# Kernel tuning notes

Hardware: AMD Instinct MI355X
Metric: run time of the kernel (lower is better)

The kernel has to match this reference:

```python
import jax, jax.numpy as jnp
import numpy as np

B, C, L = 64, 64, 8192
EPS = float(np.finfo(np.float32).eps)  # matches np.finfo(np.float32).eps in the torch code


def setup_inputs() -> dict:
    key = jax.random.key(0)
    k1, k2, k3 = jax.random.split(key, 3)
    data = jax.random.normal(k1, (B, C, L), dtype=jnp.float32)
    idxes = jax.random.randint(k2, (B, L), 0, L).astype(jnp.int32)
    # prefix lengths in [1, L] so every slice is non-empty (ragged branch)
    zero_pos = jax.random.randint(k3, (B,), 1, L + 1)
    return {"data": data, "idxes": idxes, "zero_pos": zero_pos}


def reference(data, idxes, zero_pos):
    # data: [B, C, L]; per-batch mean/std over the prefix data[b, :, :zero_pos[b]]
    Bn, Cn, Ln = data.shape
    mask = (jnp.arange(Ln)[None, :] < zero_pos[:, None])[:, None, :].astype(data.dtype)  # [B,1,L]
    cnt = Cn * zero_pos.astype(data.dtype)  # [B] number of elements in each prefix
    mean = jnp.sum(data * mask, axis=(1, 2)) / cnt  # [B]
    diff = (data - mean[:, None, None]) * mask  # [B,C,L]
    var = jnp.sum(diff * diff, axis=(1, 2)) / (cnt - 1.0)  # unbiased, as torch.std
    std = jnp.sqrt(var)  # [B]
    out = (data - mean[:, None, None]) / (std[:, None, None] + EPS)
    return (out, idxes, zero_pos)
```

## Files before the change

kernel.cpp:

```cpp
#include <hip/hip_runtime.h>
#include <math.h>

#define BB 64
#define CC 64
#define LL 8192
#define EPS_F 1.1920928955078125e-07f
#define SPLITS 32

#define NORM_BLOCKS_PER_B 64
#define NB_NORM (BB * NORM_BLOCKS_PER_B)
#define NB_AUX  512

typedef float f4 __attribute__((ext_vector_type(4)));
typedef int   i4 __attribute__((ext_vector_type(4)));


__global__ __launch_bounds__(256) void tln_stats(const float* __restrict__ data,
                          const int* __restrict__ zero_pos,
                          float2* __restrict__ partials) {
    const int b = blockIdx.x;
    const int s = blockIdx.y;
    const int tid = threadIdx.x;
    const int zp = zero_pos[b];
    const int nv = zp >> 2;
    const float* base = data + (size_t)b * CC * LL;

    float sum = 0.0f, sq = 0.0f;
    for (int c = s; c < CC; c += SPLITS) {
        const float* rowp = base + (size_t)c * LL;
        const f4* row4 = (const f4*)rowp;
        for (int i = tid; i < nv; i += 256) {
            f4 v = row4[i];
            sum += v.x + v.y + v.z + v.w;
            sq  += v.x * v.x + v.y * v.y + v.z * v.z + v.w * v.w;
        }
        for (int l = (nv << 2) + tid; l < zp; l += 256) {
            float v = rowp[l];
            sum += v;
            sq  += v * v;
        }
    }

    #pragma unroll
    for (int off = 32; off > 0; off >>= 1) {
        sum += __shfl_down(sum, off);
        sq  += __shfl_down(sq, off);
    }
    __shared__ float lsum[4], lsq[4];
    const int wave = tid >> 6;
    const int lane = tid & 63;
    if (lane == 0) { lsum[wave] = sum; lsq[wave] = sq; }
    __syncthreads();
    if (tid == 0) {
        float2 p;
        p.x = lsum[0] + lsum[1] + lsum[2] + lsum[3];
        p.y = lsq[0] + lsq[1] + lsq[2] + lsq[3];
        partials[b * SPLITS + s] = p;
    }
}

__global__ __launch_bounds__(256) void tln_fused(const f4* __restrict__ data4,
                          const float2* __restrict__ partials,
                          const int* __restrict__ zero_pos,
                          const i4* __restrict__ idxes,
                          f4* __restrict__ out4,
                          f4* __restrict__ out_idx,
                          float* __restrict__ out_zp) {
    const int blk = blockIdx.x;
    const int tid = threadIdx.x;

    if (blk < NB_NORM) {
        const int b = blk >> 6;
        const int t = blk & 63;
        const int lane = tid & 63;

        float2 p = partials[(b << 5) + (lane & 31)];
        float s_ = p.x, q_ = p.y;
        #pragma unroll
        for (int off = 16; off > 0; off >>= 1) {
            s_ += __shfl_xor(s_, off);
            q_ += __shfl_xor(q_, off);
        }
        const float cnt  = (float)CC * (float)zero_pos[b];
        const float mean = s_ / cnt;
        const float var  = (q_ - cnt * mean * mean) / (cnt - 1.0f);
        const float inv  = 1.0f / (sqrtf(var) + EPS_F);

        const size_t base = ((size_t)b << 17) | ((size_t)t << 11) | (size_t)tid;
        #pragma unroll
        for (int k = 0; k < 8; ++k) {
            const size_t i = base + ((size_t)k << 8);
            f4 v = data4[i];
            f4 o = (v - mean) * inv;
            __builtin_nontemporal_store(o, out4 + i);
        }
    } else {
        const int j = blk - NB_NORM;
        const int i = j * 256 + tid;
        i4 v = idxes[i];
        f4 o = __builtin_convertvector(v, f4);
        __builtin_nontemporal_store(o, out_idx + i);
        if (j == 0 && tid < BB) out_zp[tid] = (float)zero_pos[tid];
    }
}

extern "C" void kernel_launch(void* const* d_in, const int* in_sizes, int n_in,
                              void* d_out, int out_size, void* d_ws, size_t ws_size,
                              hipStream_t stream) {
    const float* data    = (const float*)d_in[0];
    const int* idxes     = (const int*)d_in[1];
    const int* zero_pos  = (const int*)d_in[2];

    float2* partials = (float2*)d_ws;

    float* out_data = (float*)d_out;
    float* out_idx  = out_data + (size_t)BB * CC * LL;
    float* out_zp   = out_idx + (size_t)BB * LL;

    tln_stats<<<dim3(BB, SPLITS), 256, 0, stream>>>(data, zero_pos, partials);

    tln_fused<<<NB_NORM + NB_AUX, 256, 0, stream>>>(
        (const f4*)data, partials, zero_pos, (const i4*)idxes,
        (f4*)out_data, (f4*)out_idx, out_zp);
}
```

Baseline: 248.3 us.

## Fuse stats and normalize kernels into one pass with atomic per-batch barrier

Merges the statistics kernel and the normalize kernel into a single launch. Each block reduces its four-row slice, adds the partial sums to per-batch atomic accumulators, and bumps a completion flag. It then spins until all 16 blocks of its batch have reported, and normalizes the same rows it just read, which are likely still in cache. The idx conversion work is folded into the same blocks. This removes one launch and the dependency gap between kernels, at the cost of a workspace memset, float atomics, and reliance on all blocks of a batch being co-resident to avoid deadlock.

```diff
diff --git a/kernel.cpp b/kernel.cpp
--- a/kernel.cpp
+++ b/kernel.cpp
@@ -5,39 +5,54 @@
 #define CC 64
 #define LL 8192
 #define EPS_F 1.1920928955078125e-07f
-#define SPLITS 32
 
-#define NORM_BLOCKS_PER_B 64
-#define NB_NORM (BB * NORM_BLOCKS_PER_B)
-#define NB_AUX  512
+#define GROUPS 16
+#define ROWS_PER_BLK 4
+#define NBLK (BB * GROUPS)
+#define ROW4 (LL / 4)
 
 typedef float f4 __attribute__((ext_vector_type(4)));
 typedef int   i4 __attribute__((ext_vector_type(4)));
 
 
-__global__ __launch_bounds__(256) void tln_stats(const float* __restrict__ data,
-                          const int* __restrict__ zero_pos,
-                          float2* __restrict__ partials) {
-    const int b = blockIdx.x;
-    const int s = blockIdx.y;
+__global__ __launch_bounds__(256) void tln_onepass(
+    const float* __restrict__ data,
+    const int*   __restrict__ zero_pos,
+    const i4*    __restrict__ idxes,
+    float*       __restrict__ ws,
+    f4*          __restrict__ out4,
+    f4*          __restrict__ out_idx,
+    float*       __restrict__ out_zp)
+{
+    const int blk = blockIdx.x;
     const int tid = threadIdx.x;
-    const int zp = zero_pos[b];
-    const int nv = zp >> 2;
-    const float* base = data + (size_t)b * CC * LL;
+    const int b   = blk >> 4;
+    const int t   = blk & 15;
+    const int zp  = zero_pos[b];
+    const int nv  = zp >> 2;
+    const int rem = zp & 3;
+
+    float* sums  = ws;
+    float* sqs   = ws + 64;
+    int*   flags = (int*)(ws + 128);
+
+    const float* base = data + ((size_t)b * CC + (size_t)t * ROWS_PER_BLK) * LL;
 
     float sum = 0.0f, sq = 0.0f;
-    for (int c = s; c < CC; c += SPLITS) {
-        const float* rowp = base + (size_t)c * LL;
+    #pragma unroll
+    for (int r = 0; r < ROWS_PER_BLK; ++r) {
+        const float* rowp = base + (size_t)r * LL;
         const f4* row4 = (const f4*)rowp;
         for (int i = tid; i < nv; i += 256) {
             f4 v = row4[i];
             sum += v.x + v.y + v.z + v.w;
             sq  += v.x * v.x + v.y * v.y + v.z * v.z + v.w * v.w;
         }
-        for (int l = (nv << 2) + tid; l < zp; l += 256) {
-            float v = rowp[l];
-            sum += v;
-            sq  += v * v;
+        if (rem && tid == 0) {
+            for (int e = 0; e < rem; ++e) {
+                float v = rowp[nv * 4 + e];
+                sum += v; sq += v * v;
+            }
         }
     }
 
@@ -47,60 +62,56 @@
         sq  += __shfl_down(sq, off);
     }
     __shared__ float lsum[4], lsq[4];
+    __shared__ float s_m, s_inv;
     const int wave = tid >> 6;
     const int lane = tid & 63;
     if (lane == 0) { lsum[wave] = sum; lsq[wave] = sq; }
     __syncthreads();
     if (tid == 0) {
-        float2 p;
-        p.x = lsum[0] + lsum[1] + lsum[2] + lsum[3];
-        p.y = lsq[0] + lsq[1] + lsq[2] + lsq[3];
-        partials[b * SPLITS + s] = p;
+        float bs = lsum[0] + lsum[1] + lsum[2] + lsum[3];
+        float bq = lsq[0] + lsq[1] + lsq[2] + lsq[3];
+        atomicAdd(&sums[b], bs);
+        atomicAdd(&sqs[b],  bq);
+        __hip_atomic_fetch_add(&flags[b], 1, __ATOMIC_RELEASE,
+                               __HIP_MEMORY_SCOPE_AGENT);
     }
-}
 
-__global__ __launch_bounds__(256) void tln_fused(const f4* __restrict__ data4,
-                          const float2* __restrict__ partials,
-                          const int* __restrict__ zero_pos,
-                          const i4* __restrict__ idxes,
-                          f4* __restrict__ out4,
-                          f4* __restrict__ out_idx,
-                          float* __restrict__ out_zp) {
-    const int blk = blockIdx.x;
-    const int tid = threadIdx.x;
+    if (tid < 128) {
+        const int ii = blk * 128 + tid;
+        i4 v = idxes[ii];
+        f4 o = __builtin_convertvector(v, f4);
+        __builtin_nontemporal_store(o, out_idx + ii);
+    }
+    if (blk == 0 && tid < BB) out_zp[tid] = (float)zero_pos[tid];
 
-    if (blk < NB_NORM) {
-        const int b = blk >> 6;
-        const int t = blk & 63;
-        const int lane = tid & 63;
+    if (tid == 0) {
+        while (__hip_atomic_load(&flags[b], __ATOMIC_ACQUIRE,
+                                 __HIP_MEMORY_SCOPE_AGENT) != GROUPS)
+            __builtin_amdgcn_s_sleep(1);
+        float S = __hip_atomic_load(&sums[b], __ATOMIC_RELAXED,
+                                    __HIP_MEMORY_SCOPE_AGENT);
+        float Q = __hip_atomic_load(&sqs[b], __ATOMIC_RELAXED,
+                                    __HIP_MEMORY_SCOPE_AGENT);
+        const float cnt  = (float)CC * (float)zp;
+        const float mean = S / cnt;
+        const float var  = (Q - cnt * mean * mean) / (cnt - 1.0f);
+        s_m   = mean;
+        s_inv = 1.0f / (sqrtf(var) + EPS_F);
+    }
+    __syncthreads();
+    const float m = s_m, inv = s_inv;
 
-        float2 p = partials[(b << 5) + (lane & 31)];
-        float s_ = p.x, q_ = p.y;
-        #pragma unroll
-        for (int off = 16; off > 0; off >>= 1) {
-            s_ += __shfl_xor(s_, off);
-            q_ += __shfl_xor(q_, off);
-        }
-        const float cnt  = (float)CC * (float)zero_pos[b];
-        const float mean = s_ / cnt;
-        const float var  = (q_ - cnt * mean * mean) / (cnt - 1.0f);
-        const float inv  = 1.0f / (sqrtf(var) + EPS_F);
-
-        const size_t base = ((size_t)b << 17) | ((size_t)t << 11) | (size_t)tid;
+    const f4* base4 = (const f4*)base;
+    const size_t obase = ((size_t)b * CC + (size_t)t * ROWS_PER_BLK) * ROW4;
+    #pragma unroll
+    for (int r = 0; r < ROWS_PER_BLK; ++r) {
         #pragma unroll
         for (int k = 0; k < 8; ++k) {
-            const size_t i = base + ((size_t)k << 8);
-            f4 v = data4[i];
-            f4 o = (v - mean) * inv;
-            __builtin_nontemporal_store(o, out4 + i);
+            const int i = r * ROW4 + k * 256 + tid;
+            f4 v = base4[i];
+            f4 o = (v - m) * inv;
+            __builtin_nontemporal_store(o, out4 + obase + i);
         }
-    } else {
-        const int j = blk - NB_NORM;
-        const int i = j * 256 + tid;
-        i4 v = idxes[i];
-        f4 o = __builtin_convertvector(v, f4);
-        __builtin_nontemporal_store(o, out_idx + i);
-        if (j == 0 && tid < BB) out_zp[tid] = (float)zero_pos[tid];
     }
 }
 
@@ -111,15 +122,13 @@
     const int* idxes     = (const int*)d_in[1];
     const int* zero_pos  = (const int*)d_in[2];
 
-    float2* partials = (float2*)d_ws;
-
     float* out_data = (float*)d_out;
     float* out_idx  = out_data + (size_t)BB * CC * LL;
     float* out_zp   = out_idx + (size_t)BB * LL;
 
-    tln_stats<<<dim3(BB, SPLITS), 256, 0, stream>>>(data, zero_pos, partials);
+    hipMemsetAsync(d_ws, 0, 192 * sizeof(float), stream);
 
-    tln_fused<<<NB_NORM + NB_AUX, 256, 0, stream>>>(
-        (const f4*)data, partials, zero_pos, (const i4*)idxes,
+    tln_onepass<<<NBLK, 256, 0, stream>>>(
+        data, zero_pos, (const i4*)idxes, (float*)d_ws,
         (f4*)out_data, (f4*)out_idx, out_zp);
 }
```

New measurement: 319.6 us. 1.29x slower.
